# Kernel tuning notes

Measured on AMD Instinct MI355X. Metric: run time of the kernel, lower is better.

## Reference

```python
import jax, jax.numpy as jnp
import numpy as np

R, B, N, H = 10, 8, 8192, 8          # ROIs, patients, nodes/ROI-graph, inner hidden
K = N // 2                            # TopKPooling ratio=0.5 -> ceil(0.5*N)
EPAIR = 65536                         # undirected edge pairs per patient graph
E = 2 * B * EPAIR                     # directed edges per ROI (both directions, all patients)
FIN = 4
HEADS, OH = 4, 16
SUPER_DIM = 2 * H + 3                 # (inner_layers+1)*hidden + 3 centroid coords = 19
EPS = 1e-5


def setup_inputs() -> dict:
    key = jax.random.key(0)
    ks = jax.random.split(key, 24)
    roi_x = jax.random.normal(ks[0], (R, B * N, FIN), jnp.float32)
    # within-graph undirected random edges, offset per patient
    u = jax.random.randint(ks[1], (R, B, EPAIR), 0, N)
    v = jax.random.randint(ks[2], (R, B, EPAIR), 0, N)
    off = (jnp.arange(B) * N)[None, :, None]
    src = jnp.concatenate([u + off, v + off], axis=-1).reshape(R, -1)
    dst = jnp.concatenate([v + off, u + off], axis=-1).reshape(R, -1)
    roi_edge_index = jnp.stack([src, dst], axis=1).astype(jnp.int32)  # [R, 2, E]
    centroids = jax.random.uniform(ks[3], (R, B, 3), jnp.float32) + 0.1  # nonzero -> all ROIs kept
    g = lambda k, s: jax.random.normal(k, s, jnp.float32) * 0.1
    return {
        'roi_x': roi_x,
        'roi_edge_index': roi_edge_index,
        'centroids': centroids,
        'gcn_w': g(ks[4], (R, FIN, H)),
        'gcn_b': g(ks[5], (R, H)),
        'ln_w': jnp.ones((R, H), jnp.float32),
        'ln_b': jnp.zeros((R, H), jnp.float32),
        'topk_w': g(ks[6], (R, H)),
        'gat1_w': g(ks[7], (SUPER_DIM, HEADS * OH)),
        'att_src1': g(ks[8], (HEADS, OH)),
        'att_dst1': g(ks[9], (HEADS, OH)),
        'gat1_b': g(ks[10], (HEADS * OH,)),
        'ln_o1_w': jnp.ones((HEADS * OH,), jnp.float32),
        'ln_o1_b': jnp.zeros((HEADS * OH,), jnp.float32),
        'gat2_w': g(ks[11], (HEADS * OH, OH)),
        'att_src2': g(ks[12], (1, OH)),
        'att_dst2': g(ks[13], (1, OH)),
        'gat2_b': g(ks[14], (OH,)),
        'ln_o2_w': jnp.ones((OH,), jnp.float32),
        'ln_o2_b': jnp.zeros((OH,), jnp.float32),
        'lin_w': g(ks[15], (OH, 2)),
        'lin_b': g(ks[16], (2,)),
    }


def _inner_roi(x, edges, cen, Wg, bg, wln, bln, wtk):
    """GCNConv(4,H)+ReLU -> graph-mode LayerNorm -> TopKPooling -> mean pools. x: [B*N, 4]."""
    src, dst = edges[0], edges[1]
    h = x @ Wg                                                     # [BN, H]
    # GCN symmetric norm with self loops: deg = in-degree + 1
    deg = jax.ops.segment_sum(jnp.ones((E,), x.dtype), dst, num_segments=B * N) + 1.0
    dis = deg ** -0.5
    norm = dis[src] * dis[dst]
    agg = jax.ops.segment_sum(h[src] * norm[:, None], dst, num_segments=B * N)
    h = jax.nn.relu(agg + h / deg[:, None] + bg)
    # PyG LayerNorm (mode='graph'): normalize over all nodes & channels per patient graph
    hb = h.reshape(B, N, H)
    mu = hb.mean(axis=(1, 2), keepdims=True)
    var = ((hb - mu) ** 2).mean(axis=(1, 2), keepdims=True)
    hn = (hb - mu) / jnp.sqrt(var + EPS) * wln + bln               # [B, N, H]
    res = hn.mean(axis=1)                                          # residual global_mean_pool [B, H]
    # TopKPooling: score = tanh(x.w/||w||); keep top K per graph; scale kept nodes by score
    s = jnp.tanh(jnp.einsum('bnh,h->bn', hn, wtk) / jnp.linalg.norm(wtk))
    vals, idx = jax.lax.top_k(s, K)                                # [B, K]
    sel = jnp.take_along_axis(hn, idx[:, :, None], axis=1) * vals[:, :, None]
    fv = sel.mean(axis=1)                                          # global_mean_pool after pooling
    return jnp.concatenate([res, fv, cen], axis=1)                 # [B, 19]


def _gat(x, src, dst, W, a_s, a_d, b, heads, oc):
    """PyG GATConv (self loops already included in src/dst)."""
    n = x.shape[0]
    h = (x @ W).reshape(n, heads, oc)
    es = (h * a_s).sum(-1)                                         # [n, heads]
    ed = (h * a_d).sum(-1)
    e = jax.nn.leaky_relu(es[src] + ed[dst], 0.2)                  # [E, heads]
    m = jax.ops.segment_max(e, dst, num_segments=n)
    ex = jnp.exp(e - m[dst])
    den = jax.ops.segment_sum(ex, dst, num_segments=n)
    alpha = ex / den[dst]
    out = jax.ops.segment_sum(h[src] * alpha[:, :, None], dst, num_segments=n)
    return out.reshape(n, heads * oc) + b


def _graph_ln(x, w, b):
    xb = x.reshape(B, R, -1)
    mu = xb.mean(axis=(1, 2), keepdims=True)
    var = ((xb - mu) ** 2).mean(axis=(1, 2), keepdims=True)
    return ((xb - mu) / jnp.sqrt(var + EPS) * w + b).reshape(B * R, -1)


def reference(roi_x, roi_edge_index, centroids, gcn_w, gcn_b, ln_w, ln_b, topk_w,
              gat1_w, att_src1, att_dst1, gat1_b, ln_o1_w, ln_o1_b,
              gat2_w, att_src2, att_dst2, gat2_b, ln_o2_w, ln_o2_b, lin_w, lin_b):
    feats = jax.vmap(_inner_roi)(roi_x, roi_edge_index, centroids,
                                 gcn_w, gcn_b, ln_w, ln_b, topk_w)   # [R, B, 19]
    super_x = feats.transpose(1, 0, 2).reshape(B * R, SUPER_DIM)      # patient-major node order
    # star edges 0->1..9 per patient, plus GATConv's default self loops
    pat = jnp.arange(B) * R
    sl = jnp.arange(B * R)
    ssrc = jnp.concatenate([jnp.repeat(pat, R - 1), sl])
    sdst = jnp.concatenate([(pat[:, None] + jnp.arange(1, R)).reshape(-1), sl])
    x1 = jax.nn.elu(_gat(super_x, ssrc, sdst, gat1_w, att_src1, att_dst1, gat1_b, HEADS, OH))
    x1 = _graph_ln(x1, ln_o1_w, ln_o1_b)
    x2 = jax.nn.elu(_gat(x1, ssrc, sdst, gat2_w, att_src2, att_dst2, gat2_b, 1, OH))
    x2 = _graph_ln(x2, ln_o2_w, ln_o2_b)
    pooled = x2.reshape(B, R, OH).mean(axis=1)                        # global_mean_pool
    # dropout p=0.5 is a no-op in eval mode
    return pooled @ lin_w + lin_b                                     # [B, 2]
```

## Files before the change

kernel.cpp:

```cpp
#include <hip/hip_runtime.h>
#include <hip/hip_bf16.h>
#include <math.h>

#define RR 10
#define BB 8
#define NN 8192
#define HH 8
#define BN 65536
#define EE (1u << 20)
#define EPB (EE / BB)
#define NPAIR (EPB / 2)
#define KK 4096
#define NSUP 80
#define CSRL8 17408

#define NTL(p) __builtin_nontemporal_load(p)
typedef int vi4 __attribute__((ext_vector_type(4)));

__global__ __launch_bounds__(1024)
void count_kernel(const int* __restrict__ ei, unsigned char* __restrict__ rankg,
                  unsigned char* __restrict__ Hg) {
  const int bid = blockIdx.x;
  const int rb = bid % 80;
  const int c = bid / 80;
  const int r = rb / BB;
  const int b = rb % BB;
  const int tid = threadIdx.x;

  __shared__ int hist[NN];
  for (int i = tid; i < NN; i += 1024) hist[i] = 0;
  __syncthreads();

  const int* up = ei + (size_t)r * 2u * EE + (size_t)b * EPB;
  const int* vp = ei + (size_t)r * 2u * EE + EE + (size_t)b * EPB;
  unsigned char* rk = rankg + (size_t)rb * EPB;

#pragma unroll
  for (int it = 0; it < 2; ++it) {
    int e = c * 8192 + it * 4096 + tid * 4;
    vi4 uu = NTL((const vi4*)(up + e));
    vi4 vv = NTL((const vi4*)(vp + e));
#define DO(j, U, V)                                                 \
    {                                                               \
      int r0 = atomicAdd(&hist[(V) & (NN - 1)], 1);                 \
      rk[e + (j)] = (unsigned char)r0;                              \
      int r1 = atomicAdd(&hist[(U) & (NN - 1)], 1);                 \
      rk[e + (j) + NPAIR] = (unsigned char)r1;                      \
    }
    DO(0, uu.x, vv.x) DO(1, uu.y, vv.y) DO(2, uu.z, vv.z) DO(3, uu.w, vv.w)
#undef DO
  }
  __syncthreads();

  unsigned char* hg = Hg + ((size_t)rb * 8 + c) * NN;
  for (int i = tid; i < NN; i += 1024) hg[i] = (unsigned char)hist[i];
}

__global__ __launch_bounds__(1024)
void merge_kernel(const unsigned char* __restrict__ Hg, const float* __restrict__ x,
                  unsigned short* __restrict__ qo8g, int* __restrict__ et8g,
                  float* __restrict__ zg) {
  const int bid = blockIdx.x;
  const int rb = bid % 80;
  const int p = bid / 80;
  const int r = rb / BB;
  const int b = rb % BB;
  const int tid = threadIdx.x;

  __shared__ int ps[1024];
  int n = p * 1024 + tid;
  const unsigned char* hg = Hg + (size_t)rb * 8 * NN;
  int deg = 0;
#pragma unroll
  for (int c = 0; c < 8; ++c) deg += (int)hg[(size_t)c * NN + n];

  ps[tid] = deg;
  __syncthreads();
  for (int s2 = 1; s2 < 1024; s2 <<= 1) {
    int v = 0;
    if (tid >= s2) v = ps[tid - s2];
    __syncthreads();
    ps[tid] += v;
    __syncthreads();
  }
  int incl = ps[tid];
  qo8g[(size_t)rb * 8192 + (size_t)p * 1024 + tid] = (unsigned short)(incl - deg);
  if (tid == 1023) et8g[rb * 8 + p] = incl;

  const float4* x4 = (const float4*)x + (size_t)r * BN + (size_t)b * NN;
  float4* z4 = (float4*)zg + (size_t)rb * NN;
  float ds = rsqrtf((float)deg + 1.0f);
  float4 xv = x4[n];
  z4[n] = make_float4(xv.x * ds, xv.y * ds, xv.z * ds, xv.w * ds);
}

__global__ __launch_bounds__(512)
void scatfuse_kernel(const int* __restrict__ ei, const float* __restrict__ zg,
                     const unsigned char* __restrict__ rankg,
                     const unsigned short* __restrict__ qo8g, const int* __restrict__ et8g,
                     const unsigned char* __restrict__ Hg,
                     const float* __restrict__ gcn_w, const float* __restrict__ gcn_b,
                     const float* __restrict__ ln_w, const float* __restrict__ topk_w,
                     float* __restrict__ v4g, float* __restrict__ tg,
                     double* __restrict__ partsS, float* __restrict__ partsC) {
  const int bid = blockIdx.x;
  const int rb = bid % 80;
  const int e8 = bid / 80;
  const int r = rb / BB;
  const int b = rb % BB;
  const int tid = threadIdx.x;

  __shared__ unsigned short qoE[1025];
  __shared__ unsigned short qoCur[1024];
  __shared__ __align__(16) unsigned short csrL[CSRL8];

  const unsigned short* qo8 = qo8g + (size_t)rb * 8192 + (size_t)e8 * 1024;
  for (int i = tid; i < 1024; i += 512) {
    unsigned short v = qo8[i];
    qoE[i] = v;
    qoCur[i] = v;
  }
  if (tid == 0) qoE[1024] = (unsigned short)et8g[rb * 8 + e8];
  __syncthreads();

  const int* up = ei + (size_t)r * 2u * EE + (size_t)b * EPB;
  const int* vp = ei + (size_t)r * 2u * EE + EE + (size_t)b * EPB;
  const unsigned char* rk = rankg + (size_t)rb * EPB;
  const unsigned char* hg = Hg + (size_t)rb * 8 * NN + (size_t)e8 * 1024;

#define SCAT(U, V, RA, RB2)                                         \
  {                                                                 \
    int lv = (V) & (NN - 1);                                        \
    if ((lv >> 10) == e8) {                                         \
      csrL[(int)qoCur[lv & 1023] + (int)(RA)] =                     \
          (unsigned short)((U) & (NN - 1));                         \
    }                                                               \
    int lu = (U) & (NN - 1);                                        \
    if ((lu >> 10) == e8) {                                         \
      csrL[(int)qoCur[lu & 1023] + (int)(RB2)] =                    \
          (unsigned short)((V) & (NN - 1));                         \
    }                                                               \
  }
  for (int c = 0; c < 8; ++c) {
#pragma unroll
    for (int it = 0; it < 4; ++it) {
      int e = c * 8192 + it * 2048 + tid * 4;
      unsigned ra = NTL((const unsigned*)(rk + e));
      unsigned rbv = NTL((const unsigned*)(rk + NPAIR + e));
      vi4 uu = NTL((const vi4*)(up + e));
      vi4 vv = NTL((const vi4*)(vp + e));
      SCAT(uu.x, vv.x, ra & 255u, rbv & 255u)
      SCAT(uu.y, vv.y, (ra >> 8) & 255u, (rbv >> 8) & 255u)
      SCAT(uu.z, vv.z, (ra >> 16) & 255u, (rbv >> 16) & 255u)
      SCAT(uu.w, vv.w, (ra >> 24) & 255u, (rbv >> 24) & 255u)
    }
    __syncthreads();
    for (int i = tid; i < 1024; i += 512)
      qoCur[i] = (unsigned short)((int)qoCur[i] + (int)hg[(size_t)c * NN + i]);
    __syncthreads();
  }
#undef SCAT

  const float* wp = gcn_w + r * 32;
  const float* bgp = gcn_b + r * 8;
  float lwwt[8];
#pragma unroll
  for (int c = 0; c < 8; ++c) lwwt[c] = ln_w[r * 8 + c] * topk_w[r * 8 + c];

  const float4* z4 = (const float4*)zg + (size_t)rb * NN;
  float4* v4o = (float4*)v4g + (size_t)rb * NN;
  float* trow = tg + (size_t)rb * NN;

  double s1 = 0.0, s2 = 0.0;
  float ch[8] = {0, 0, 0, 0, 0, 0, 0, 0};

#pragma unroll
  for (int k = 0; k < 2; ++k) {
    int idx = tid + k * 512;
    int n = e8 * 1024 + idx;
    int o = (int)qoE[idx];
    int c = (int)qoE[idx + 1] - o;
    float4 zn = z4[n];
    float sx = zn.x, sy = zn.y, sz = zn.z, sw = zn.w;
    int j = 0;
    for (; j + 3 < c; j += 4) {
      int n0 = csrL[o + j], n1 = csrL[o + j + 1], n2 = csrL[o + j + 2], n3 = csrL[o + j + 3];
      float4 a0 = z4[n0], a1 = z4[n1], a2 = z4[n2], a3 = z4[n3];
      sx += a0.x + a1.x + a2.x + a3.x;
      sy += a0.y + a1.y + a2.y + a3.y;
      sz += a0.z + a1.z + a2.z + a3.z;
      sw += a0.w + a1.w + a2.w + a3.w;
    }
    for (; j < c; ++j) {
      int n0 = csrL[o + j];
      float4 a0 = z4[n0];
      sx += a0.x; sy += a0.y; sz += a0.z; sw += a0.w;
    }
    float dd = rsqrtf((float)c + 1.0f);
    float v0 = sx * dd, v1 = sy * dd, v2 = sz * dd, v3 = sw * dd;
    v4o[n] = make_float4(v0, v1, v2, v3);
    float t = 0.f;
#pragma unroll
    for (int cc = 0; cc < 8; ++cc) {
      float h = fmaxf(v0 * wp[cc] + v1 * wp[8 + cc] + v2 * wp[16 + cc] + v3 * wp[24 + cc] + bgp[cc], 0.0f);
      s1 += h;
      s2 += (double)h * h;
      ch[cc] += h;
      t += h * lwwt[cc];
    }
    trow[n] = t;
  }

  __syncthreads();
  double* wredS = (double*)csrL;
  float* wredC = (float*)(csrL + 512);
  int lane = tid & 63, wid = tid >> 6;
#pragma unroll
  for (int off = 32; off > 0; off >>= 1) {
    s1 += __shfl_down(s1, off);
    s2 += __shfl_down(s2, off);
#pragma unroll
    for (int cc = 0; cc < 8; ++cc) ch[cc] += __shfl_down(ch[cc], off);
  }
  if (lane == 0) {
    wredS[wid * 2] = s1;
    wredS[wid * 2 + 1] = s2;
#pragma unroll
    for (int cc = 0; cc < 8; ++cc) wredC[wid * 8 + cc] = ch[cc];
  }
  __syncthreads();
  if (tid == 0) {
    double a = 0.0, b3 = 0.0;
    for (int w2 = 0; w2 < 8; ++w2) { a += wredS[w2 * 2]; b3 += wredS[w2 * 2 + 1]; }
    partsS[bid * 2] = a;
    partsS[bid * 2 + 1] = b3;
  }
  if (tid < 8) {
    float sc = 0.f;
    for (int w2 = 0; w2 < 8; ++w2) sc += wredC[w2 * 8 + tid];
    partsC[bid * 8 + tid] = sc;
  }
}

__global__ __launch_bounds__(1024)
void roiB_kernel(const float* __restrict__ tg, const float* __restrict__ v4g,
                 const double* __restrict__ partsS, const float* __restrict__ partsC,
                 const float* __restrict__ gcn_w, const float* __restrict__ gcn_b,
                 const float* __restrict__ ln_w, const float* __restrict__ ln_b,
                 const float* __restrict__ topk_w, const float* __restrict__ cen,
                 float* __restrict__ feats) {
  const int rb = blockIdx.x;
  const int r = rb / BB;
  const int tid = threadIdx.x;
  const int lane = tid & 63, wid = tid >> 6;

  __shared__ int histW[16 * 256];
  __shared__ int wtot[16];
  __shared__ float chS[8];
  __shared__ float fvSum[8];
  __shared__ int cntGt;
  __shared__ int selb, kleft;
  __shared__ float sstat[2];

  float lw[8], lb[8], wt[8], w[32], bg[8];
  float wn2 = 0.f, L1 = 0.f, B1 = 0.f;
#pragma unroll
  for (int i = 0; i < 32; ++i) w[i] = gcn_w[r * 32 + i];
#pragma unroll
  for (int c = 0; c < 8; ++c) {
    lw[c] = ln_w[r * 8 + c];
    lb[c] = ln_b[r * 8 + c];
    wt[c] = topk_w[r * 8 + c];
    bg[c] = gcn_b[r * 8 + c];
    wn2 += wt[c] * wt[c];
    L1 += lw[c] * wt[c];
    B1 += lb[c] * wt[c];
  }
  const float invn = 1.0f / sqrtf(wn2);

  if (tid == 0) {
    double s1 = 0.0, s2 = 0.0;
    for (int p = 0; p < 8; ++p) {
      s1 += partsS[(p * 80 + rb) * 2];
      s2 += partsS[(p * 80 + rb) * 2 + 1];
    }
    const double M = (double)NN * HH;
    double mu = s1 / M;
    double var = s2 / M - mu * mu;
    sstat[0] = (float)mu;
    sstat[1] = (float)(1.0 / sqrt(var + 1e-5));
    cntGt = 0;
  }
  if (tid < 8) {
    float sc = 0.f;
    for (int p = 0; p < 8; ++p) sc += partsC[(p * 80 + rb) * 8 + tid];
    chS[tid] = sc;
    fvSum[tid] = 0.f;
  }
  __syncthreads();
  const float muf = sstat[0];
  const float rstd = sstat[1];
  const float C0 = B1 - rstd * muf * L1;

  const float* trow = tg + (size_t)rb * NN;
  float sv[8];
  unsigned fl[8];
#pragma unroll
  for (int i = 0; i < 8; ++i) {
    int n = tid * 8 + i;
    float s = tanhf((rstd * trow[n] + C0) * invn);
    sv[i] = s;
    unsigned u = __float_as_uint(s);
    fl[i] = (u & 0x80000000u) ? ~u : (u | 0x80000000u);
  }

  unsigned prefix = 0;
  int kneed = KK;
  for (int shift = 24; shift >= 0; shift -= 8) {
#pragma unroll
    for (int z = 0; z < 4; ++z) histW[tid + z * 1024] = 0;
    __syncthreads();
#pragma unroll
    for (int i = 0; i < 8; ++i) {
      bool m = (shift == 24) || ((fl[i] >> (shift + 8)) == prefix);
      if (m) atomicAdd(&histW[wid * 256 + ((fl[i] >> shift) & 255)], 1);
    }
    __syncthreads();
    if (wid == 0) {
      int b0 = lane * 4;
      int t0 = 0, t1 = 0, t2 = 0, t3 = 0;
      for (int w2 = 0; w2 < 16; ++w2) {
        const int* hp2 = &histW[w2 * 256 + b0];
        t0 += hp2[0]; t1 += hp2[1]; t2 += hp2[2]; t3 += hp2[3];
      }
      int s3 = t3, s2i = t2 + s3, s1i = t1 + s2i, s0 = t0 + s1i;
      int v = s0;
#pragma unroll
      for (int off = 1; off < 64; off <<= 1) {
        int o = __shfl_down(v, off);
        v += (lane + off < 64) ? o : 0;
      }
      int above = v - s0;
      int S3 = above + s3, S2 = above + s2i, S1 = above + s1i, S0 = above + s0;
      if (S3 >= kneed && above < kneed)      { selb = b0 + 3; kleft = kneed - above; }
      else if (S2 >= kneed && S3 < kneed)    { selb = b0 + 2; kleft = kneed - S3; }
      else if (S1 >= kneed && S2 < kneed)    { selb = b0 + 1; kleft = kneed - S2; }
      else if (S0 >= kneed && S1 < kneed)    { selb = b0;     kleft = kneed - S1; }
    }
    __syncthreads();
    prefix = (prefix << 8) | (unsigned)selb;
    kneed = kleft;
  }
  float tau = (prefix & 0x80000000u) ? __uint_as_float(prefix & 0x7fffffffu)
                                     : __uint_as_float(~prefix);

  int cg = 0, ct = 0;
#pragma unroll
  for (int i = 0; i < 8; ++i) {
    if (sv[i] > tau) cg++;
    else if (sv[i] == tau) ct++;
  }
  int wcg = cg;
#pragma unroll
  for (int off = 32; off > 0; off >>= 1) wcg += __shfl_down(wcg, off);
  if (lane == 0) atomicAdd(&cntGt, wcg);
  int sc = ct;
#pragma unroll
  for (int off = 1; off < 64; off <<= 1) {
    int o = __shfl_up(sc, off);
    if (lane >= off) sc += o;
  }
  if (lane == 63) wtot[wid] = sc;
  __syncthreads();
  int wbase = 0;
  for (int w2 = 0; w2 < wid; ++w2) wbase += wtot[w2];
  int rank = wbase + sc - ct;
  int quota = KK - cntGt;

  const float4* v4r = (const float4*)v4g + (size_t)rb * NN;
  float fva[8] = {0, 0, 0, 0, 0, 0, 0, 0};
#pragma unroll
  for (int i = 0; i < 8; ++i) {
    bool inc = sv[i] > tau;
    if (!inc && sv[i] == tau) { inc = (rank < quota); rank++; }
    if (inc) {
      int n = tid * 8 + i;
      float4 vv = v4r[n];
#pragma unroll
      for (int c = 0; c < 8; ++c) {
        float h = fmaxf(vv.x * w[c] + vv.y * w[8 + c] + vv.z * w[16 + c] + vv.w * w[24 + c] + bg[c], 0.0f);
        float hn = (h - muf) * rstd * lw[c] + lb[c];
        fva[c] += hn * sv[i];
      }
    }
  }
#pragma unroll
  for (int c = 0; c < 8; ++c) atomicAdd(&fvSum[c], fva[c]);
  __syncthreads();

  size_t fo = (size_t)rb * 19;
  if (tid < 8) {
    feats[fo + tid] = ((chS[tid] - (float)NN * muf) * rstd * lw[tid]) / (float)NN + lb[tid];
    feats[fo + 8 + tid] = fvSum[tid] / (float)KK;
  }
  if (tid >= 16 && tid < 19) {
    feats[fo + tid] = cen[(size_t)rb * 3 + (tid - 16)];
  }
}

__global__ __launch_bounds__(256)
void super_kernel(const float* __restrict__ feats,
                  const float* __restrict__ W1, const float* __restrict__ as1,
                  const float* __restrict__ ad1, const float* __restrict__ b1,
                  const float* __restrict__ lnw1, const float* __restrict__ lnb1,
                  const float* __restrict__ W2, const float* __restrict__ as2,
                  const float* __restrict__ ad2, const float* __restrict__ b2,
                  const float* __restrict__ lnw2, const float* __restrict__ lnb2,
                  const float* __restrict__ linw, const float* __restrict__ linb,
                  float* __restrict__ out) {
  __shared__ float sx[NSUP * 19];
  __shared__ float h1[NSUP * 64];
  __shared__ float x1[NSUP * 64];
  __shared__ float es1[NSUP * 4], ed1[NSUP * 4];
  __shared__ float h2[NSUP * 16], x2[NSUP * 16];
  __shared__ float es2[NSUP], ed2[NSUP];
  __shared__ float stat[16];
  const int tid = threadIdx.x;

  for (int i = tid; i < NSUP * 19; i += 256) {
    int n = i / 19, c = i % 19;
    int bb = n / RR, rr = n % RR;
    sx[i] = feats[(size_t)(rr * BB + bb) * 19 + c];
  }
  __syncthreads();
  for (int p = tid; p < NSUP * 64; p += 256) {
    int n = p / 64, j = p % 64;
    float acc = 0.f;
    for (int k2 = 0; k2 < 19; ++k2) acc += sx[n * 19 + k2] * W1[k2 * 64 + j];
    h1[p] = acc;
  }
  __syncthreads();
  for (int p = tid; p < NSUP * 4; p += 256) {
    int n = p / 4, hd = p % 4;
    float a = 0.f, d2 = 0.f;
    for (int o = 0; o < 16; ++o) {
      float hv = h1[n * 64 + hd * 16 + o];
      a += hv * as1[hd * 16 + o];
      d2 += hv * ad1[hd * 16 + o];
    }
    es1[p] = a; ed1[p] = d2;
  }
  __syncthreads();
  for (int p = tid; p < NSUP * 64; p += 256) {
    int n = p / 64, j = p % 64, hd = j / 16;
    int rr = n % RR;
    float o;
    if (rr == 0) {
      o = h1[p];
    } else {
      int hub = n - rr;
      float eh = es1[hub * 4 + hd] + ed1[n * 4 + hd];
      float esf = es1[n * 4 + hd] + ed1[n * 4 + hd];
      eh = eh > 0.f ? eh : 0.2f * eh;
      esf = esf > 0.f ? esf : 0.2f * esf;
      float m = fmaxf(eh, esf);
      float wh = expf(eh - m), ws2 = expf(esf - m);
      o = (wh * h1[hub * 64 + j] + ws2 * h1[n * 64 + j]) / (wh + ws2);
    }
    float v = o + b1[j];
    x1[p] = v > 0.f ? v : expm1f(v);
  }
  __syncthreads();
  if (tid < BB) {
    double m = 0.0, v2 = 0.0;
    for (int q = 0; q < RR * 64; ++q) {
      float val = x1[tid * RR * 64 + q];
      m += val; v2 += (double)val * val;
    }
    m /= (RR * 64.0); v2 = v2 / (RR * 64.0) - m * m;
    stat[tid] = (float)m;
    stat[8 + tid] = (float)(1.0 / sqrt(v2 + 1e-5));
  }
  __syncthreads();
  for (int p = tid; p < NSUP * 64; p += 256) {
    int n = p / 64, j = p % 64, bb = n / RR;
    x1[p] = (x1[p] - stat[bb]) * stat[8 + bb] * lnw1[j] + lnb1[j];
  }
  __syncthreads();
  for (int p = tid; p < NSUP * 16; p += 256) {
    int n = p / 16, o = p % 16;
    float acc = 0.f;
    for (int j = 0; j < 64; ++j) acc += x1[n * 64 + j] * W2[j * 16 + o];
    h2[p] = acc;
  }
  __syncthreads();
  for (int n = tid; n < NSUP; n += 256) {
    float a = 0.f, d2 = 0.f;
    for (int o = 0; o < 16; ++o) {
      float hv = h2[n * 16 + o];
      a += hv * as2[o];
      d2 += hv * ad2[o];
    }
    es2[n] = a; ed2[n] = d2;
  }
  __syncthreads();
  for (int p = tid; p < NSUP * 16; p += 256) {
    int n = p / 16, o = p % 16;
    int rr = n % RR;
    float ov;
    if (rr == 0) ov = h2[p];
    else {
      int hub = n - rr;
      float eh = es2[hub] + ed2[n];
      float esf = es2[n] + ed2[n];
      eh = eh > 0.f ? eh : 0.2f * eh;
      esf = esf > 0.f ? esf : 0.2f * esf;
      float m = fmaxf(eh, esf);
      float wh = expf(eh - m), ws2 = expf(esf - m);
      ov = (wh * h2[hub * 16 + o] + ws2 * h2[p]) / (wh + ws2);
    }
    float v = ov + b2[o];
    x2[p] = v > 0.f ? v : expm1f(v);
  }
  __syncthreads();
  if (tid < BB) {
    double m = 0.0, v2 = 0.0;
    for (int q = 0; q < RR * 16; ++q) {
      float val = x2[tid * RR * 16 + q];
      m += val; v2 += (double)val * val;
    }
    m /= (RR * 16.0); v2 = v2 / (RR * 16.0) - m * m;
    stat[tid] = (float)m;
    stat[8 + tid] = (float)(1.0 / sqrt(v2 + 1e-5));
  }
  __syncthreads();
  for (int p = tid; p < NSUP * 16; p += 256) {
    int n = p / 16, o = p % 16, bb = n / RR;
    x2[p] = (x2[p] - stat[bb]) * stat[8 + bb] * lnw2[o] + lnb2[o];
  }
  __syncthreads();
  if (tid < BB * 2) {
    int bb = tid / 2, t = tid % 2;
    float acc = linb[t];
    for (int o = 0; o < 16; ++o) {
      float pm = 0.f;
      for (int rr = 0; rr < RR; ++rr) pm += x2[(bb * RR + rr) * 16 + o];
      pm /= (float)RR;
      acc += pm * linw[o * 2 + t];
    }
    out[bb * 2 + t] = acc;
  }
}

extern "C" void kernel_launch(void* const* d_in, const int* in_sizes, int n_in,
                              void* d_out, int out_size, void* d_ws, size_t ws_size,
                              hipStream_t stream) {
  const float* roi_x = (const float*)d_in[0];
  const int* ei = (const int*)d_in[1];
  const float* cen = (const float*)d_in[2];
  const float* gcn_w = (const float*)d_in[3];
  const float* gcn_b = (const float*)d_in[4];
  const float* ln_w = (const float*)d_in[5];
  const float* ln_b = (const float*)d_in[6];
  const float* topk_w = (const float*)d_in[7];
  const float* gat1_w = (const float*)d_in[8];
  const float* as1 = (const float*)d_in[9];
  const float* ad1 = (const float*)d_in[10];
  const float* b1 = (const float*)d_in[11];
  const float* lnw1 = (const float*)d_in[12];
  const float* lnb1 = (const float*)d_in[13];
  const float* W2 = (const float*)d_in[14];
  const float* as2 = (const float*)d_in[15];
  const float* ad2 = (const float*)d_in[16];
  const float* b2 = (const float*)d_in[17];
  const float* lnw2 = (const float*)d_in[18];
  const float* lnb2 = (const float*)d_in[19];
  const float* linw = (const float*)d_in[20];
  const float* linb = (const float*)d_in[21];
  float* out = (float*)d_out;

  char* wsb = (char*)d_ws;
  float* v4g = (float*)wsb;
  float* zg = (float*)(wsb + (size_t)80 * NN * 4 * 4);
  float* tg = (float*)((char*)zg + (size_t)80 * NN * 4 * 4);
  double* partsS = (double*)((char*)tg + (size_t)80 * NN * 4);
  float* partsC = (float*)((char*)partsS + 1280 * 8);
  unsigned short* qo8 = (unsigned short*)((char*)partsC + 5120 * 4);
  int* et8 = (int*)((char*)qo8 + (size_t)80 * 8192 * 2);
  float* feats = (float*)((char*)et8 + 640 * 4);
  unsigned char* rankg = (unsigned char*)((char*)feats + (size_t)RR * BB * 19 * 4);
  unsigned char* Hg = rankg + (size_t)80 * EPB;

  count_kernel<<<640, 1024, 0, stream>>>(ei, rankg, Hg);
  merge_kernel<<<640, 1024, 0, stream>>>(Hg, roi_x, qo8, et8, zg);
  scatfuse_kernel<<<640, 512, 0, stream>>>(ei, zg, rankg, qo8, et8, Hg,
                                           gcn_w, gcn_b, ln_w, topk_w,
                                           v4g, tg, partsS, partsC);
  roiB_kernel<<<80, 1024, 0, stream>>>(tg, v4g, partsS, partsC,
                                       gcn_w, gcn_b, ln_w, ln_b, topk_w, cen, feats);
  super_kernel<<<1, 256, 0, stream>>>(feats, gat1_w, as1, ad1, b1, lnw1, lnb1,
                                      W2, as2, ad2, b2, lnw2, lnb2, linw, linb, out);
}
```

Measured before the change: 181.0 us.

## Precompute per-chunk exclusive histogram prefix to remove per-chunk barriers in scatter

merge_kernel now rewrites the per-chunk degree histograms in place as exclusive running sums across the 8 edge chunks. scatfuse_kernel loads these into an 8KB shared table and computes each CSR slot as base offset plus chunk prefix plus rank, with no shared cursor to update. This drops the 16 __syncthreads and cursor-update passes from the scatter loop so it becomes one unrolled 32-iteration stream. The cost is more shared memory and an extra global write of Hg in merge_kernel.

Result: no change. 181.0 us (+0.0%).

```diff
diff --git a/kernel.cpp b/kernel.cpp
--- a/kernel.cpp
+++ b/kernel.cpp
@@ -57,7 +57,7 @@
 }
 
 __global__ __launch_bounds__(1024)
-void merge_kernel(const unsigned char* __restrict__ Hg, const float* __restrict__ x,
+void merge_kernel(unsigned char* __restrict__ Hg, const float* __restrict__ x,
                   unsigned short* __restrict__ qo8g, int* __restrict__ et8g,
                   float* __restrict__ zg) {
   const int bid = blockIdx.x;
@@ -69,10 +69,17 @@
 
   __shared__ int ps[1024];
   int n = p * 1024 + tid;
-  const unsigned char* hg = Hg + (size_t)rb * 8 * NN;
+  unsigned char* hg = Hg + (size_t)rb * 8 * NN;
+  unsigned char h[8];
   int deg = 0;
 #pragma unroll
-  for (int c = 0; c < 8; ++c) deg += (int)hg[(size_t)c * NN + n];
+  for (int c = 0; c < 8; ++c) { h[c] = hg[(size_t)c * NN + n]; deg += (int)h[c]; }
+  int run = 0;
+#pragma unroll
+  for (int c = 0; c < 8; ++c) {
+    hg[(size_t)c * NN + n] = (unsigned char)run;
+    run += (int)h[c];
+  }
 
   ps[tid] = deg;
   __syncthreads();
@@ -111,55 +118,53 @@
   const int tid = threadIdx.x;
 
   __shared__ unsigned short qoE[1025];
-  __shared__ unsigned short qoCur[1024];
+  __shared__ unsigned char cumL[8192];
   __shared__ __align__(16) unsigned short csrL[CSRL8];
 
   const unsigned short* qo8 = qo8g + (size_t)rb * 8192 + (size_t)e8 * 1024;
-  for (int i = tid; i < 1024; i += 512) {
-    unsigned short v = qo8[i];
-    qoE[i] = v;
-    qoCur[i] = v;
-  }
+  for (int i = tid; i < 1024; i += 512) qoE[i] = qo8[i];
   if (tid == 0) qoE[1024] = (unsigned short)et8g[rb * 8 + e8];
+  const unsigned char* hg = Hg + (size_t)rb * 8 * NN + (size_t)e8 * 1024;
+  for (int i = tid; i < 8192; i += 512) {
+    int c = i >> 10, nn = i & 1023;
+    cumL[i] = hg[(size_t)c * NN + nn];
+  }
   __syncthreads();
 
   const int* up = ei + (size_t)r * 2u * EE + (size_t)b * EPB;
   const int* vp = ei + (size_t)r * 2u * EE + EE + (size_t)b * EPB;
   const unsigned char* rk = rankg + (size_t)rb * EPB;
-  const unsigned char* hg = Hg + (size_t)rb * 8 * NN + (size_t)e8 * 1024;
-
-#define SCAT(U, V, RA, RB2)                                         \
+
+#define SCAT(U, V, RA, RB2, CB)                                     \
   {                                                                 \
     int lv = (V) & (NN - 1);                                        \
     if ((lv >> 10) == e8) {                                         \
-      csrL[(int)qoCur[lv & 1023] + (int)(RA)] =                     \
+      int d = lv & 1023;                                            \
+      csrL[(int)qoE[d] + (int)cumL[(CB) | d] + (int)(RA)] =         \
           (unsigned short)((U) & (NN - 1));                         \
     }                                                               \
     int lu = (U) & (NN - 1);                                        \
     if ((lu >> 10) == e8) {                                         \
-      csrL[(int)qoCur[lu & 1023] + (int)(RB2)] =                    \
+      int d = lu & 1023;                                            \
+      csrL[(int)qoE[d] + (int)cumL[(CB) | d] + (int)(RB2)] =        \
           (unsigned short)((V) & (NN - 1));                         \
     }                                                               \
   }
-  for (int c = 0; c < 8; ++c) {
-#pragma unroll
-    for (int it = 0; it < 4; ++it) {
-      int e = c * 8192 + it * 2048 + tid * 4;
-      unsigned ra = NTL((const unsigned*)(rk + e));
-      unsigned rbv = NTL((const unsigned*)(rk + NPAIR + e));
-      vi4 uu = NTL((const vi4*)(up + e));
-      vi4 vv = NTL((const vi4*)(vp + e));
-      SCAT(uu.x, vv.x, ra & 255u, rbv & 255u)
-      SCAT(uu.y, vv.y, (ra >> 8) & 255u, (rbv >> 8) & 255u)
-      SCAT(uu.z, vv.z, (ra >> 16) & 255u, (rbv >> 16) & 255u)
-      SCAT(uu.w, vv.w, (ra >> 24) & 255u, (rbv >> 24) & 255u)
-    }
-    __syncthreads();
-    for (int i = tid; i < 1024; i += 512)
-      qoCur[i] = (unsigned short)((int)qoCur[i] + (int)hg[(size_t)c * NN + i]);
-    __syncthreads();
+#pragma unroll 4
+  for (int it = 0; it < 32; ++it) {
+    int e = it * 2048 + tid * 4;
+    int cb = (it >> 2) << 10;
+    unsigned ra = NTL((const unsigned*)(rk + e));
+    unsigned rbv = NTL((const unsigned*)(rk + NPAIR + e));
+    vi4 uu = NTL((const vi4*)(up + e));
+    vi4 vv = NTL((const vi4*)(vp + e));
+    SCAT(uu.x, vv.x, ra & 255u, rbv & 255u, cb)
+    SCAT(uu.y, vv.y, (ra >> 8) & 255u, (rbv >> 8) & 255u, cb)
+    SCAT(uu.z, vv.z, (ra >> 16) & 255u, (rbv >> 16) & 255u, cb)
+    SCAT(uu.w, vv.w, (ra >> 24) & 255u, (rbv >> 24) & 255u, cb)
   }
 #undef SCAT
+  __syncthreads();
 
   const float* wp = gcn_w + r * 32;
   const float* bgp = gcn_b + r * 8;
```

## Replace CSR build and gather with LDS float-atomic scatter aggregation

Applied to the files above, without the earlier changes.

Drops the rank/prefix-sum CSR construction and the CSR gather. Each block now scatter-adds neighbour features into a 128KB LDS accumulator with float atomics, split across two halves of each graph's edges, and a new final kernel combines the two partial sums with normalization and the GCN epilogue. This removes the rank array traffic and the serial scan, at the cost of eight LDS float atomics per edge. It also cuts grid parallelism for the accumulate stage to 160 blocks and makes the summation order nondeterministic.

New measurement: 442.5 us. +144.5%, slower.

```diff
diff --git a/kernel.cpp b/kernel.cpp
--- a/kernel.cpp
+++ b/kernel.cpp
@@ -12,14 +12,12 @@
 #define NPAIR (EPB / 2)
 #define KK 4096
 #define NSUP 80
-#define CSRL8 17408
 
 #define NTL(p) __builtin_nontemporal_load(p)
 typedef int vi4 __attribute__((ext_vector_type(4)));
 
 __global__ __launch_bounds__(1024)
-void count_kernel(const int* __restrict__ ei, unsigned char* __restrict__ rankg,
-                  unsigned char* __restrict__ Hg) {
+void count_kernel(const int* __restrict__ ei, unsigned char* __restrict__ Hg) {
   const int bid = blockIdx.x;
   const int rb = bid % 80;
   const int c = bid / 80;
@@ -33,22 +31,16 @@
 
   const int* up = ei + (size_t)r * 2u * EE + (size_t)b * EPB;
   const int* vp = ei + (size_t)r * 2u * EE + EE + (size_t)b * EPB;
-  unsigned char* rk = rankg + (size_t)rb * EPB;
 
 #pragma unroll
   for (int it = 0; it < 2; ++it) {
     int e = c * 8192 + it * 4096 + tid * 4;
     vi4 uu = NTL((const vi4*)(up + e));
     vi4 vv = NTL((const vi4*)(vp + e));
-#define DO(j, U, V)                                                 \
-    {                                                               \
-      int r0 = atomicAdd(&hist[(V) & (NN - 1)], 1);                 \
-      rk[e + (j)] = (unsigned char)r0;                              \
-      int r1 = atomicAdd(&hist[(U) & (NN - 1)], 1);                 \
-      rk[e + (j) + NPAIR] = (unsigned char)r1;                      \
-    }
-    DO(0, uu.x, vv.x) DO(1, uu.y, vv.y) DO(2, uu.z, vv.z) DO(3, uu.w, vv.w)
-#undef DO
+    atomicAdd(&hist[vv.x & (NN - 1)], 1); atomicAdd(&hist[uu.x & (NN - 1)], 1);
+    atomicAdd(&hist[vv.y & (NN - 1)], 1); atomicAdd(&hist[uu.y & (NN - 1)], 1);
+    atomicAdd(&hist[vv.z & (NN - 1)], 1); atomicAdd(&hist[uu.z & (NN - 1)], 1);
+    atomicAdd(&hist[vv.w & (NN - 1)], 1); atomicAdd(&hist[uu.w & (NN - 1)], 1);
   }
   __syncthreads();
 
@@ -58,34 +50,19 @@
 
 __global__ __launch_bounds__(1024)
 void merge_kernel(const unsigned char* __restrict__ Hg, const float* __restrict__ x,
-                  unsigned short* __restrict__ qo8g, int* __restrict__ et8g,
-                  float* __restrict__ zg) {
+                  unsigned char* __restrict__ degg, float* __restrict__ zg) {
   const int bid = blockIdx.x;
   const int rb = bid % 80;
   const int p = bid / 80;
   const int r = rb / BB;
   const int b = rb % BB;
-  const int tid = threadIdx.x;
-
-  __shared__ int ps[1024];
-  int n = p * 1024 + tid;
+  const int n = p * 1024 + threadIdx.x;
+
   const unsigned char* hg = Hg + (size_t)rb * 8 * NN;
   int deg = 0;
 #pragma unroll
   for (int c = 0; c < 8; ++c) deg += (int)hg[(size_t)c * NN + n];
-
-  ps[tid] = deg;
-  __syncthreads();
-  for (int s2 = 1; s2 < 1024; s2 <<= 1) {
-    int v = 0;
-    if (tid >= s2) v = ps[tid - s2];
-    __syncthreads();
-    ps[tid] += v;
-    __syncthreads();
-  }
-  int incl = ps[tid];
-  qo8g[(size_t)rb * 8192 + (size_t)p * 1024 + tid] = (unsigned short)(incl - deg);
-  if (tid == 1023) et8g[rb * 8 + p] = incl;
+  degg[(size_t)rb * NN + n] = (unsigned char)deg;
 
   const float4* x4 = (const float4*)x + (size_t)r * BN + (size_t)b * NN;
   float4* z4 = (float4*)zg + (size_t)rb * NN;
@@ -94,72 +71,71 @@
   z4[n] = make_float4(xv.x * ds, xv.y * ds, xv.z * ds, xv.w * ds);
 }
 
-__global__ __launch_bounds__(512)
-void scatfuse_kernel(const int* __restrict__ ei, const float* __restrict__ zg,
-                     const unsigned char* __restrict__ rankg,
-                     const unsigned short* __restrict__ qo8g, const int* __restrict__ et8g,
-                     const unsigned char* __restrict__ Hg,
-                     const float* __restrict__ gcn_w, const float* __restrict__ gcn_b,
-                     const float* __restrict__ ln_w, const float* __restrict__ topk_w,
-                     float* __restrict__ v4g, float* __restrict__ tg,
-                     double* __restrict__ partsS, float* __restrict__ partsC) {
+__global__ __launch_bounds__(1024)
+void accum_kernel(const int* __restrict__ ei, const float* __restrict__ zg,
+                  float* __restrict__ P0, float* __restrict__ P1) {
   const int bid = blockIdx.x;
   const int rb = bid % 80;
-  const int e8 = bid / 80;
+  const int h = bid / 80;
   const int r = rb / BB;
   const int b = rb % BB;
   const int tid = threadIdx.x;
 
-  __shared__ unsigned short qoE[1025];
-  __shared__ unsigned short qoCur[1024];
-  __shared__ __align__(16) unsigned short csrL[CSRL8];
-
-  const unsigned short* qo8 = qo8g + (size_t)rb * 8192 + (size_t)e8 * 1024;
-  for (int i = tid; i < 1024; i += 512) {
-    unsigned short v = qo8[i];
-    qoE[i] = v;
-    qoCur[i] = v;
-  }
-  if (tid == 0) qoE[1024] = (unsigned short)et8g[rb * 8 + e8];
+  __shared__ float acc[4 * NN];
+  for (int i = tid; i < 4 * NN; i += 1024) acc[i] = 0.f;
   __syncthreads();
 
   const int* up = ei + (size_t)r * 2u * EE + (size_t)b * EPB;
   const int* vp = ei + (size_t)r * 2u * EE + EE + (size_t)b * EPB;
-  const unsigned char* rk = rankg + (size_t)rb * EPB;
-  const unsigned char* hg = Hg + (size_t)rb * 8 * NN + (size_t)e8 * 1024;
-
-#define SCAT(U, V, RA, RB2)                                         \
-  {                                                                 \
-    int lv = (V) & (NN - 1);                                        \
-    if ((lv >> 10) == e8) {                                         \
-      csrL[(int)qoCur[lv & 1023] + (int)(RA)] =                     \
-          (unsigned short)((U) & (NN - 1));                         \
-    }                                                               \
-    int lu = (U) & (NN - 1);                                        \
-    if ((lu >> 10) == e8) {                                         \
-      csrL[(int)qoCur[lu & 1023] + (int)(RB2)] =                    \
-          (unsigned short)((V) & (NN - 1));                         \
-    }                                                               \
-  }
-  for (int c = 0; c < 8; ++c) {
-#pragma unroll
-    for (int it = 0; it < 4; ++it) {
-      int e = c * 8192 + it * 2048 + tid * 4;
-      unsigned ra = NTL((const unsigned*)(rk + e));
-      unsigned rbv = NTL((const unsigned*)(rk + NPAIR + e));
-      vi4 uu = NTL((const vi4*)(up + e));
-      vi4 vv = NTL((const vi4*)(vp + e));
-      SCAT(uu.x, vv.x, ra & 255u, rbv & 255u)
-      SCAT(uu.y, vv.y, (ra >> 8) & 255u, (rbv >> 8) & 255u)
-      SCAT(uu.z, vv.z, (ra >> 16) & 255u, (rbv >> 16) & 255u)
-      SCAT(uu.w, vv.w, (ra >> 24) & 255u, (rbv >> 24) & 255u)
-    }
-    __syncthreads();
-    for (int i = tid; i < 1024; i += 512)
-      qoCur[i] = (unsigned short)((int)qoCur[i] + (int)hg[(size_t)c * NN + i]);
-    __syncthreads();
-  }
-#undef SCAT
+  const float4* z4 = (const float4*)zg + (size_t)rb * NN;
+
+#pragma unroll
+  for (int it = 0; it < 8; ++it) {
+    int e = h * 32768 + it * 4096 + tid * 4;
+    vi4 uu = NTL((const vi4*)(up + e));
+    vi4 vv = NTL((const vi4*)(vp + e));
+#define DO(U, V)                                                    \
+    {                                                               \
+      int su = (U) & (NN - 1), dv = (V) & (NN - 1);                 \
+      float4 zu = z4[su];                                           \
+      atomicAdd(&acc[dv], zu.x);                                    \
+      atomicAdd(&acc[NN + dv], zu.y);                               \
+      atomicAdd(&acc[2 * NN + dv], zu.z);                           \
+      atomicAdd(&acc[3 * NN + dv], zu.w);                           \
+      float4 zv = z4[dv];                                           \
+      atomicAdd(&acc[su], zv.x);                                    \
+      atomicAdd(&acc[NN + su], zv.y);                               \
+      atomicAdd(&acc[2 * NN + su], zv.z);                           \
+      atomicAdd(&acc[3 * NN + su], zv.w);                           \
+    }
+    DO(uu.x, vv.x) DO(uu.y, vv.y) DO(uu.z, vv.z) DO(uu.w, vv.w)
+#undef DO
+  }
+  __syncthreads();
+
+  float* Ph = (h ? P1 : P0) + (size_t)rb * NN * 4;
+  for (int n = tid; n < NN; n += 1024) {
+    float4 v = make_float4(acc[n], acc[NN + n], acc[2 * NN + n], acc[3 * NN + n]);
+    ((float4*)Ph)[n] = v;
+  }
+}
+
+__global__ __launch_bounds__(1024)
+void final_kernel(float* __restrict__ P0, const float* __restrict__ P1,
+                  const float* __restrict__ zg, const unsigned char* __restrict__ degg,
+                  const float* __restrict__ gcn_w, const float* __restrict__ gcn_b,
+                  const float* __restrict__ ln_w, const float* __restrict__ topk_w,
+                  float* __restrict__ tg, double* __restrict__ partsS,
+                  float* __restrict__ partsC) {
+  const int bid = blockIdx.x;
+  const int rb = bid % 80;
+  const int p = bid / 80;
+  const int r = rb / BB;
+  const int tid = threadIdx.x;
+  const int n = p * 1024 + tid;
+
+  __shared__ double wredS[16 * 2];
+  __shared__ float wredC[16 * 8];
 
   const float* wp = gcn_w + r * 32;
   const float* bgp = gcn_b + r * 8;
@@ -167,53 +143,31 @@
 #pragma unroll
   for (int c = 0; c < 8; ++c) lwwt[c] = ln_w[r * 8 + c] * topk_w[r * 8 + c];
 
+  float4* p0 = (float4*)P0 + (size_t)rb * NN;
+  const float4* p1 = (const float4*)P1 + (size_t)rb * NN;
   const float4* z4 = (const float4*)zg + (size_t)rb * NN;
-  float4* v4o = (float4*)v4g + (size_t)rb * NN;
-  float* trow = tg + (size_t)rb * NN;
+
+  float4 a = p0[n], b4 = p1[n], zn = z4[n];
+  float dd = rsqrtf((float)degg[(size_t)rb * NN + n] + 1.0f);
+  float v0 = dd * (a.x + b4.x + zn.x);
+  float v1 = dd * (a.y + b4.y + zn.y);
+  float v2 = dd * (a.z + b4.z + zn.z);
+  float v3 = dd * (a.w + b4.w + zn.w);
+  p0[n] = make_float4(v0, v1, v2, v3);
 
   double s1 = 0.0, s2 = 0.0;
-  float ch[8] = {0, 0, 0, 0, 0, 0, 0, 0};
-
-#pragma unroll
-  for (int k = 0; k < 2; ++k) {
-    int idx = tid + k * 512;
-    int n = e8 * 1024 + idx;
-    int o = (int)qoE[idx];
-    int c = (int)qoE[idx + 1] - o;
-    float4 zn = z4[n];
-    float sx = zn.x, sy = zn.y, sz = zn.z, sw = zn.w;
-    int j = 0;
-    for (; j + 3 < c; j += 4) {
-      int n0 = csrL[o + j], n1 = csrL[o + j + 1], n2 = csrL[o + j + 2], n3 = csrL[o + j + 3];
-      float4 a0 = z4[n0], a1 = z4[n1], a2 = z4[n2], a3 = z4[n3];
-      sx += a0.x + a1.x + a2.x + a3.x;
-      sy += a0.y + a1.y + a2.y + a3.y;
-      sz += a0.z + a1.z + a2.z + a3.z;
-      sw += a0.w + a1.w + a2.w + a3.w;
-    }
-    for (; j < c; ++j) {
-      int n0 = csrL[o + j];
-      float4 a0 = z4[n0];
-      sx += a0.x; sy += a0.y; sz += a0.z; sw += a0.w;
-    }
-    float dd = rsqrtf((float)c + 1.0f);
-    float v0 = sx * dd, v1 = sy * dd, v2 = sz * dd, v3 = sw * dd;
-    v4o[n] = make_float4(v0, v1, v2, v3);
-    float t = 0.f;
-#pragma unroll
-    for (int cc = 0; cc < 8; ++cc) {
-      float h = fmaxf(v0 * wp[cc] + v1 * wp[8 + cc] + v2 * wp[16 + cc] + v3 * wp[24 + cc] + bgp[cc], 0.0f);
-      s1 += h;
-      s2 += (double)h * h;
-      ch[cc] += h;
-      t += h * lwwt[cc];
-    }
-    trow[n] = t;
-  }
-
-  __syncthreads();
-  double* wredS = (double*)csrL;
-  float* wredC = (float*)(csrL + 512);
+  float ch[8];
+  float t = 0.f;
+#pragma unroll
+  for (int cc = 0; cc < 8; ++cc) {
+    float hv = fmaxf(v0 * wp[cc] + v1 * wp[8 + cc] + v2 * wp[16 + cc] + v3 * wp[24 + cc] + bgp[cc], 0.0f);
+    ch[cc] = hv;
+    s1 += hv;
+    s2 += (double)hv * hv;
+    t += hv * lwwt[cc];
+  }
+  tg[(size_t)rb * NN + n] = t;
+
   int lane = tid & 63, wid = tid >> 6;
 #pragma unroll
   for (int off = 32; off > 0; off >>= 1) {
@@ -230,14 +184,14 @@
   }
   __syncthreads();
   if (tid == 0) {
-    double a = 0.0, b3 = 0.0;
-    for (int w2 = 0; w2 < 8; ++w2) { a += wredS[w2 * 2]; b3 += wredS[w2 * 2 + 1]; }
-    partsS[bid * 2] = a;
-    partsS[bid * 2 + 1] = b3;
+    double aa = 0.0, bb2 = 0.0;
+    for (int w2 = 0; w2 < 16; ++w2) { aa += wredS[w2 * 2]; bb2 += wredS[w2 * 2 + 1]; }
+    partsS[bid * 2] = aa;
+    partsS[bid * 2 + 1] = bb2;
   }
   if (tid < 8) {
     float sc = 0.f;
-    for (int w2 = 0; w2 < 8; ++w2) sc += wredC[w2 * 8 + tid];
+    for (int w2 = 0; w2 < 16; ++w2) sc += wredC[w2 * 8 + tid];
     partsC[bid * 8 + tid] = sc;
   }
 }
@@ -580,23 +534,22 @@
   float* out = (float*)d_out;
 
   char* wsb = (char*)d_ws;
-  float* v4g = (float*)wsb;
-  float* zg = (float*)(wsb + (size_t)80 * NN * 4 * 4);
-  float* tg = (float*)((char*)zg + (size_t)80 * NN * 4 * 4);
-  double* partsS = (double*)((char*)tg + (size_t)80 * NN * 4);
+  float* P0 = (float*)wsb;
+  float* P1 = P0 + (size_t)80 * NN * 4;
+  float* zg = P1 + (size_t)80 * NN * 4;
+  float* tg = zg + (size_t)80 * NN * 4;
+  double* partsS = (double*)(tg + (size_t)80 * NN);
   float* partsC = (float*)((char*)partsS + 1280 * 8);
-  unsigned short* qo8 = (unsigned short*)((char*)partsC + 5120 * 4);
-  int* et8 = (int*)((char*)qo8 + (size_t)80 * 8192 * 2);
-  float* feats = (float*)((char*)et8 + 640 * 4);
-  unsigned char* rankg = (unsigned char*)((char*)feats + (size_t)RR * BB * 19 * 4);
-  unsigned char* Hg = rankg + (size_t)80 * EPB;
-
-  count_kernel<<<640, 1024, 0, stream>>>(ei, rankg, Hg);
-  merge_kernel<<<640, 1024, 0, stream>>>(Hg, roi_x, qo8, et8, zg);
-  scatfuse_kernel<<<640, 512, 0, stream>>>(ei, zg, rankg, qo8, et8, Hg,
-                                           gcn_w, gcn_b, ln_w, topk_w,
-                                           v4g, tg, partsS, partsC);
-  roiB_kernel<<<80, 1024, 0, stream>>>(tg, v4g, partsS, partsC,
+  unsigned char* degg = (unsigned char*)((char*)partsC + 5120 * 4);
+  unsigned char* Hg = degg + (size_t)80 * NN;
+  float* feats = (float*)(Hg + (size_t)80 * 8 * NN);
+
+  count_kernel<<<640, 1024, 0, stream>>>(ei, Hg);
+  merge_kernel<<<640, 1024, 0, stream>>>(Hg, roi_x, degg, zg);
+  accum_kernel<<<160, 1024, 0, stream>>>(ei, zg, P0, P1);
+  final_kernel<<<640, 1024, 0, stream>>>(P0, P1, zg, degg, gcn_w, gcn_b, ln_w, topk_w,
+                                         tg, partsS, partsC);
+  roiB_kernel<<<80, 1024, 0, stream>>>(tg, P0 , partsS, partsC,
                                        gcn_w, gcn_b, ln_w, ln_b, topk_w, cen, feats);
   super_kernel<<<1, 256, 0, stream>>>(feats, gat1_w, as1, ad1, b1, lnw1, lnb1,
                                       W2, as2, ad2, b2, lnw2, lnb2, linw, linb, out);
```
